# Optimization experiments

Hardware: AMD Instinct MI355X
Metric: run time of the kernel (lower is better)

The kernel has to match this reference:

```python
import jax, jax.numpy as jnp
import numpy as np

B, C, N, DI, DC = 64, 32, 1152, 8, 16
ROUTINGS = 3


def squash(x, axis=-1):
    sq = jnp.sum(x * x, axis=axis, keepdims=True)
    scale = sq / (1.0 + sq) / jnp.sqrt(sq + 1e-07)
    return scale * x


def setup_inputs() -> dict:
    key = jax.random.key(0)
    k1, k2 = jax.random.split(key)
    inputs = jax.random.normal(k1, (B, N, DI), dtype=jnp.float32)
    # Xavier-uniform init for W[n_caps, n_in, d_cap, d_in]; fan computed over last two dims
    limit = float(np.sqrt(6.0 / (DC + DI)))
    W = jax.random.uniform(k2, (C, N, DC, DI), dtype=jnp.float32, minval=-limit, maxval=limit)
    return {"inputs": inputs, "W": W}


def reference(inputs, W):
    # inputs_hat[b,c,n,i] = sum_j W[c,n,i,j] * inputs[b,n,j]
    inputs_hat = jnp.einsum('cnij,bnj->bcni', W, inputs)  # [B,C,N,DC]
    b = jnp.zeros((B, C, N), dtype=inputs_hat.dtype)
    outputs = None
    for i in range(ROUTINGS):
        c = jax.nn.softmax(b, axis=1)                      # over output capsules
        s = jnp.einsum('bcn,bcni->bci', c, inputs_hat)     # weighted sum over input caps
        outputs = squash(s)                                # [B,C,DC]
        if i < ROUTINGS - 1:
            agreement = jnp.einsum('bci,bcni->bcn', outputs, inputs_hat)
            b = b + agreement
    return outputs
```

## Files before the change

### kernel.cpp

```cpp
#include <hip/hip_runtime.h>
#include <hip/hip_fp16.h>

#define B_  64
#define C_  32
#define N_  1152
#define DI_ 8
#define DC_ 16
#define NCH 3
#define NSLOT 128
#define STH 512
#define NOCT 16

static __device__ __forceinline__ unsigned pkh(float a, float b) {
    __half2 t = __float22half2_rn(make_float2(a, b));
    return *reinterpret_cast<unsigned*>(&t);
}
static __device__ __forceinline__ float2 uph(unsigned u) {
    __half2 h; *reinterpret_cast<unsigned*>(&h) = u;
    return __half22float2(h);
}

__global__ __launch_bounds__(STH, 2) void caps_hat(
    const float* __restrict__ X, const float* __restrict__ W,
    uint4* __restrict__ hatg, float* __restrict__ p1)
{
    __shared__ float wlds[NCH * 64 * 64];
    __shared__ float xlds[NCH * 16 * 8];

    const int bg   = blockIdx.x & 3;
    const int slot = blockIdx.x >> 2;
    const int tid  = threadIdx.x;
    const int w    = tid >> 6;
    const int lane = tid & 63;
    const int c    = lane & 31;
    const int h    = lane >> 5;
    const int bl0  = w * 2;
    const int le   = 2 * c + h;
    const int sw   = c & 7;

    float acc[2][8];
#pragma unroll
    for (int bq = 0; bq < 2; bq++)
#pragma unroll
        for (int r = 0; r < 8; r++) acc[bq][r] = 0.f;

    for (int cc = 0; cc < 3; cc++) {
        if (cc) __syncthreads();
        const int n0 = (slot + cc * NSLOT) * NCH;

        for (int G = tid; G < NCH * 1024; G += STH) {
            const int nl = G >> 10, f = (G >> 4) & 63, q = G & 15;
            const int wc = f >> 1, wh = f & 1;
            const float4 v = *(const float4*)(W + (size_t)(wc * N_ + n0 + nl) * 128 + wh * 64 + q * 4);
            *(float4*)(wlds + (nl * 64 + f) * 64 + (q ^ (wc & 7)) * 4) = v;
        }
        if (tid < NCH * 32) {
            const int nl = tid >> 5, bl = (tid >> 1) & 15, qx = tid & 1;
            const float4 v = *(const float4*)(X + (size_t)((bg * 16 + bl) * N_ + n0 + nl) * DI_ + qx * 4);
            *(float4*)(xlds + (nl * 16 + bl) * 8 + qx * 4) = v;
        }
        __syncthreads();

#pragma unroll
        for (int nl = 0; nl < NCH; nl++) {
            float4 xa[2], xb[2];
#pragma unroll
            for (int bq = 0; bq < 2; bq++) {
                const float* xp = xlds + (nl * 16 + bl0 + bq) * 8;
                xa[bq] = *(const float4*)xp;
                xb[bq] = *(const float4*)(xp + 4);
            }
            uint4 hq[2];
            const float* frag = wlds + (nl * 64 + le) * 64;
#pragma unroll
            for (int rp = 0; rp < 4; rp++) {
                const int r0 = 2 * rp, r1 = r0 + 1;
                const int pa0 = ((2 * r0) ^ sw) * 4;
                const int pb0 = pa0 ^ 4;
                const int pa1 = ((2 * r1) ^ sw) * 4;
                const int pb1 = pa1 ^ 4;
                const float4 wa0 = *(const float4*)(frag + pa0);
                const float4 wb0 = *(const float4*)(frag + pb0);
                const float4 wa1 = *(const float4*)(frag + pa1);
                const float4 wb1 = *(const float4*)(frag + pb1);
#pragma unroll
                for (int bq = 0; bq < 2; bq++) {
                    const float hv0 = wa0.x*xa[bq].x + wa0.y*xa[bq].y + wa0.z*xa[bq].z + wa0.w*xa[bq].w
                                    + wb0.x*xb[bq].x + wb0.y*xb[bq].y + wb0.z*xb[bq].z + wb0.w*xb[bq].w;
                    const float hv1 = wa1.x*xa[bq].x + wa1.y*xa[bq].y + wa1.z*xa[bq].z + wa1.w*xa[bq].w
                                    + wb1.x*xb[bq].x + wb1.y*xb[bq].y + wb1.z*xb[bq].z + wb1.w*xb[bq].w;
                    acc[bq][r0] += hv0;
                    acc[bq][r1] += hv1;
                    (&hq[bq].x)[rp] = pkh(hv0, hv1);
                }
            }
#pragma unroll
            for (int bq = 0; bq < 2; bq++) {
                const int b = bg * 16 + bl0 + bq;
                hatg[(size_t)(b * N_ + n0 + nl) * 64 + le] = hq[bq];
            }
        }
    }

    float* pout = p1 + (size_t)(bg * NSLOT + slot) * 8192;
#pragma unroll
    for (int bq = 0; bq < 2; bq++) {
        float* pb = pout + (bl0 + bq) * 512 + le * 8;
        *(float4*)pb       = make_float4(acc[bq][0]*0.03125f, acc[bq][1]*0.03125f,
                                         acc[bq][2]*0.03125f, acc[bq][3]*0.03125f);
        *(float4*)(pb + 4) = make_float4(acc[bq][4]*0.03125f, acc[bq][5]*0.03125f,
                                         acc[bq][6]*0.03125f, acc[bq][7]*0.03125f);
    }
}

__global__ __launch_bounds__(STH, 2) void caps_route(
    const uint4* __restrict__ hatg, const float* __restrict__ accb,
    float* __restrict__ p2)
{
    __shared__ float red[8 * 512];
    const int b    = blockIdx.x >> 4;
    const int oct  = blockIdx.x & 15;
    const int tid  = threadIdx.x;
    const int w    = tid >> 6;
    const int lane = tid & 63;
    const int c    = lane & 31;
    const int h    = lane >> 5;
    const int le   = 2 * c + h;

    const float* ap = accb + (size_t)b * 512 + le * 8;
    const float4 a0 = *(const float4*)ap;
    const float4 a1 = *(const float4*)(ap + 4);

    float acc[8] = {0.f,0.f,0.f,0.f,0.f,0.f,0.f,0.f};
    const uint4* hb = hatg + (size_t)(b * N_ + oct * 72) * 64 + le;

    uint4 v[2][3];
#pragma unroll
    for (int u = 0; u < 3; u++)
        v[0][u] = hb[(size_t)(w + 8 * u) * 64];

#pragma unroll
    for (int k = 0; k < 3; k++) {
        const int cur = k & 1, nxt = cur ^ 1;
        if (k < 2) {
#pragma unroll
            for (int u = 0; u < 3; u++)
                v[nxt][u] = hb[(size_t)(w + 8 * (3 * (k + 1) + u)) * 64];
        }
#pragma unroll
        for (int u = 0; u < 3; u++) {
            const float2 f0 = uph(v[cur][u].x);
            const float2 f1 = uph(v[cur][u].y);
            const float2 f2 = uph(v[cur][u].z);
            const float2 f3 = uph(v[cur][u].w);
            float lg = f0.x*a0.x + f0.y*a0.y + f1.x*a0.z + f1.y*a0.w
                     + f2.x*a1.x + f2.y*a1.y + f3.x*a1.z + f3.y*a1.w;
            lg += __shfl_xor(lg, 32, 64);
            const float e = __expf(lg);
            float s = e;
#pragma unroll
            for (int m = 16; m >= 1; m >>= 1) s += __shfl_xor(s, m, 64);
            const float sc = e * __builtin_amdgcn_rcpf(s);
            acc[0] += sc * f0.x; acc[1] += sc * f0.y;
            acc[2] += sc * f1.x; acc[3] += sc * f1.y;
            acc[4] += sc * f2.x; acc[5] += sc * f2.y;
            acc[6] += sc * f3.x; acc[7] += sc * f3.y;
        }
    }
    *(float4*)(red + w * 512 + le * 8)     = make_float4(acc[0], acc[1], acc[2], acc[3]);
    *(float4*)(red + w * 512 + le * 8 + 4) = make_float4(acc[4], acc[5], acc[6], acc[7]);
    __syncthreads();
    float vs = 0.f;
#pragma unroll
    for (int s = 0; s < 8; s++) vs += red[s * 512 + tid];
    p2[(size_t)(b * NOCT + oct) * 512 + tid] = vs;
}

__global__ __launch_bounds__(256) void caps_r1(
    const float* __restrict__ p1, float* __restrict__ accb,
    float* __restrict__ out, int t)
{
    const int b   = blockIdx.x >> 2;
    const int q   = blockIdx.x & 3;
    const int tid = threadIdx.x;
    const int e   = q * 128 + (tid >> 1);
    const int p   = tid & 1;
    const int bg  = b >> 4, bl = b & 15;
    const float* base = p1 + (size_t)bg * NSLOT * 8192 + (size_t)bl * 512 + e;
    float v = 0.f;
#pragma unroll 8
    for (int ch = p; ch < NSLOT; ch += 2)
        v += base[(size_t)ch * 8192];
    v += __shfl_xor(v, 1, 64);
    float sq = v * v;
#pragma unroll
    for (int m = 2; m <= 16; m <<= 1) sq += __shfl_xor(sq, m, 64);
    const float scale = sq / (1.f + sq) * rsqrtf(sq + 1e-7f);
    const float ov = v * scale;
    if (p == 0) {
        const int oidx = b * 512 + e;
        if (t == 2) out[oidx] = ov;
        else        accb[oidx] = (t == 0) ? ov : (accb[oidx] + ov);
    }
}

__global__ __launch_bounds__(512) void caps_r2(
    const float* __restrict__ p2, float* __restrict__ accb,
    float* __restrict__ out, int t)
{
    const int b = blockIdx.x;
    const int e = threadIdx.x;
    const float* base = p2 + (size_t)b * (NOCT * 512) + e;
    float v = 0.f;
#pragma unroll
    for (int s = 0; s < NOCT; s++) v += base[s * 512];
    float sq = v * v;
#pragma unroll
    for (int m = 1; m <= 8; m <<= 1) sq += __shfl_xor(sq, m, 64);
    const float scale = sq / (1.f + sq) * rsqrtf(sq + 1e-7f);
    const float ov = v * scale;
    const int oidx = b * 512 + e;
    if (t == 2) out[oidx] = ov;
    else        accb[oidx] += ov;
}

__global__ __launch_bounds__(STH, 2) void caps_s_fb(
    const float* __restrict__ X, const float* __restrict__ W,
    const float* __restrict__ aout, float* __restrict__ partials, int t)
{
    __shared__ float wlds[NCH * 64 * 64];
    __shared__ float xlds[NCH * 16 * 8];
    const int bg = blockIdx.x & 3, slot = blockIdx.x >> 2;
    const int tid = threadIdx.x, w = tid >> 6, lane = tid & 63;
    const int c = lane & 31, h = lane >> 5, bl0 = w * 2, sw = c & 7;
    float areg[2][8] = {};
    if (t > 0) {
#pragma unroll
        for (int bq = 0; bq < 2; bq++) {
            const float* ap = aout + (size_t)(bg * 16 + bl0 + bq) * 512 + c * 16 + h * 8;
            const float4 a0 = *(const float4*)ap; const float4 a1 = *(const float4*)(ap + 4);
            areg[bq][0]=a0.x; areg[bq][1]=a0.y; areg[bq][2]=a0.z; areg[bq][3]=a0.w;
            areg[bq][4]=a1.x; areg[bq][5]=a1.y; areg[bq][6]=a1.z; areg[bq][7]=a1.w;
        }
    }
    float acc[2][8];
#pragma unroll
    for (int bq = 0; bq < 2; bq++)
#pragma unroll
        for (int r = 0; r < 8; r++) acc[bq][r] = 0.f;
    for (int cc = 0; cc < 3; cc++) {
        if (cc) __syncthreads();
        const int n0 = (slot + cc * NSLOT) * NCH;
        for (int G = tid; G < NCH * 1024; G += STH) {
            const int nl = G >> 10, f = (G >> 4) & 63, q = G & 15;
            const int wc = f >> 1, wh = f & 1;
            const float4 v = *(const float4*)(W + (size_t)(wc * N_ + n0 + nl) * 128 + wh * 64 + q * 4);
            *(float4*)(wlds + (nl * 64 + f) * 64 + (q ^ (wc & 7)) * 4) = v;
        }
        if (tid < NCH * 32) {
            const int nl = tid >> 5, bl = (tid >> 1) & 15, qx = tid & 1;
            const float4 v = *(const float4*)(X + (size_t)((bg * 16 + bl) * N_ + n0 + nl) * DI_ + qx * 4);
            *(float4*)(xlds + (nl * 16 + bl) * 8 + qx * 4) = v;
        }
        __syncthreads();
#pragma unroll
        for (int nl = 0; nl < NCH; nl++) {
            float4 xa[2], xb[2];
#pragma unroll
            for (int bq = 0; bq < 2; bq++) {
                const float* xp = xlds + (nl * 16 + bl0 + bq) * 8;
                xa[bq] = *(const float4*)xp; xb[bq] = *(const float4*)(xp + 4);
            }
            float hat[2][8];
            const float* frag = wlds + (nl * 64 + 2 * c + h) * 64;
#pragma unroll
            for (int r = 0; r < 8; r++) {
                const int pa = ((2 * r) ^ sw) * 4; const int pb = pa ^ 4;
                const float4 wa = *(const float4*)(frag + pa);
                const float4 wb = *(const float4*)(frag + pb);
#pragma unroll
                for (int bq = 0; bq < 2; bq++)
                    hat[bq][r] = wa.x*xa[bq].x + wa.y*xa[bq].y + wa.z*xa[bq].z + wa.w*xa[bq].w
                               + wb.x*xb[bq].x + wb.y*xb[bq].y + wb.z*xb[bq].z + wb.w*xb[bq].w;
            }
#pragma unroll
            for (int bq = 0; bq < 2; bq++) {
                float softc;
                if (t > 0) {
                    float lg = hat[bq][0]*areg[bq][0] + hat[bq][1]*areg[bq][1]
                             + hat[bq][2]*areg[bq][2] + hat[bq][3]*areg[bq][3]
                             + hat[bq][4]*areg[bq][4] + hat[bq][5]*areg[bq][5]
                             + hat[bq][6]*areg[bq][6] + hat[bq][7]*areg[bq][7];
                    lg += __shfl_xor(lg, 32, 64);
                    const float e = __expf(lg);
                    float s = e;
#pragma unroll
                    for (int m = 16; m >= 1; m >>= 1) s += __shfl_xor(s, m, 64);
                    softc = e / s;
                } else softc = 1.0f / 32.0f;
#pragma unroll
                for (int r = 0; r < 8; r++) acc[bq][r] += softc * hat[bq][r];
            }
        }
    }
    float* pout = partials + (size_t)(bg * NSLOT + slot) * 8192;
#pragma unroll
    for (int bq = 0; bq < 2; bq++) {
        float* pb = pout + (bl0 + bq) * 512 + c * 16 + h * 8;
        *(float4*)pb       = make_float4(acc[bq][0], acc[bq][1], acc[bq][2], acc[bq][3]);
        *(float4*)(pb + 4) = make_float4(acc[bq][4], acc[bq][5], acc[bq][6], acc[bq][7]);
    }
}

extern "C" void kernel_launch(void* const* d_in, const int* in_sizes, int n_in,
                              void* d_out, int out_size, void* d_ws, size_t ws_size,
                              hipStream_t stream) {
    const float* X = (const float*)d_in[0];
    const float* W = (const float*)d_in[1];
    float* out = (float*)d_out;

    const size_t hat_b = (size_t)B_ * N_ * 512 * 2;
    const size_t p1_b  = (size_t)512 * 8192 * 4;
    const size_t p2_b  = (size_t)B_ * NOCT * 512 * 4;
    const size_t acc_b = (size_t)B_ * 512 * 4;

    if (ws_size >= hat_b + p1_b + p2_b + acc_b) {
        char* ws = (char*)d_ws;
        uint4* hatg = (uint4*)ws;
        float* p1   = (float*)(ws + hat_b);
        float* p2   = (float*)(ws + hat_b + p1_b);
        float* accb = (float*)(ws + hat_b + p1_b + p2_b);
        caps_hat  <<<512, STH, 0, stream>>>(X, W, hatg, p1);
        caps_r1   <<<256, 256, 0, stream>>>(p1, accb, out, 0);
        caps_route<<<B_ * NOCT, STH, 0, stream>>>(hatg, accb, p2);
        caps_r2   <<<64, 512, 0, stream>>>(p2, accb, out, 1);
        caps_route<<<B_ * NOCT, STH, 0, stream>>>(hatg, accb, p2);
        caps_r2   <<<64, 512, 0, stream>>>(p2, accb, out, 2);
    } else {
        float* p1 = (float*)d_ws;
        float* accb = p1 + (size_t)512 * 8192;
        for (int t = 0; t < 3; t++) {
            caps_s_fb<<<512, STH, 0, stream>>>(X, W, accb, p1, t);
            caps_r1  <<<256, 256, 0, stream>>>(p1, accb, out, t);
        }
    }
}
```

Before: 140.0 us.

## Simplify hat kernel to per-input-capsule blocks and route first iteration from fp16 hat

The hat kernel is rewritten so each 64-thread block handles one input capsule, keeping its W slice in registers and looping over all 64 batches. It no longer writes the large fp32 partial-sum buffer. The first routing iteration now reuses the route kernel in a uniform-weight mode reading the stored fp16 hat, with a postscale of 1/32. This drops the p1 write and the reduction kernel in exchange for one extra pass over hat and a tiny-block launch of 1152 blocks. The route kernel also issues all nine loads up front instead of double-buffering them.

```diff
diff --git a/kernel.cpp b/kernel.cpp
--- a/kernel.cpp
+++ b/kernel.cpp
@@ -20,102 +20,51 @@
     return __half22float2(h);
 }
 
-__global__ __launch_bounds__(STH, 2) void caps_hat(
+__global__ __launch_bounds__(64) void caps_hat(
     const float* __restrict__ X, const float* __restrict__ W,
-    uint4* __restrict__ hatg, float* __restrict__ p1)
-{
-    __shared__ float wlds[NCH * 64 * 64];
-    __shared__ float xlds[NCH * 16 * 8];
-
-    const int bg   = blockIdx.x & 3;
-    const int slot = blockIdx.x >> 2;
-    const int tid  = threadIdx.x;
-    const int w    = tid >> 6;
-    const int lane = tid & 63;
+    uint4* __restrict__ hatg)
+{
+    __shared__ float xl[64 * 8];
+    const int n    = blockIdx.x;
+    const int lane = threadIdx.x;
     const int c    = lane & 31;
     const int h    = lane >> 5;
-    const int bl0  = w * 2;
-    const int le   = 2 * c + h;
-    const int sw   = c & 7;
-
-    float acc[2][8];
-#pragma unroll
-    for (int bq = 0; bq < 2; bq++)
-#pragma unroll
-        for (int r = 0; r < 8; r++) acc[bq][r] = 0.f;
-
-    for (int cc = 0; cc < 3; cc++) {
-        if (cc) __syncthreads();
-        const int n0 = (slot + cc * NSLOT) * NCH;
-
-        for (int G = tid; G < NCH * 1024; G += STH) {
-            const int nl = G >> 10, f = (G >> 4) & 63, q = G & 15;
-            const int wc = f >> 1, wh = f & 1;
-            const float4 v = *(const float4*)(W + (size_t)(wc * N_ + n0 + nl) * 128 + wh * 64 + q * 4);
-            *(float4*)(wlds + (nl * 64 + f) * 64 + (q ^ (wc & 7)) * 4) = v;
-        }
-        if (tid < NCH * 32) {
-            const int nl = tid >> 5, bl = (tid >> 1) & 15, qx = tid & 1;
-            const float4 v = *(const float4*)(X + (size_t)((bg * 16 + bl) * N_ + n0 + nl) * DI_ + qx * 4);
-            *(float4*)(xlds + (nl * 16 + bl) * 8 + qx * 4) = v;
-        }
-        __syncthreads();
-
-#pragma unroll
-        for (int nl = 0; nl < NCH; nl++) {
-            float4 xa[2], xb[2];
-#pragma unroll
-            for (int bq = 0; bq < 2; bq++) {
-                const float* xp = xlds + (nl * 16 + bl0 + bq) * 8;
-                xa[bq] = *(const float4*)xp;
-                xb[bq] = *(const float4*)(xp + 4);
-            }
-            uint4 hq[2];
-            const float* frag = wlds + (nl * 64 + le) * 64;
-#pragma unroll
-            for (int rp = 0; rp < 4; rp++) {
-                const int r0 = 2 * rp, r1 = r0 + 1;
-                const int pa0 = ((2 * r0) ^ sw) * 4;
-                const int pb0 = pa0 ^ 4;
-                const int pa1 = ((2 * r1) ^ sw) * 4;
-                const int pb1 = pa1 ^ 4;
-                const float4 wa0 = *(const float4*)(frag + pa0);
-                const float4 wb0 = *(const float4*)(frag + pb0);
-                const float4 wa1 = *(const float4*)(frag + pa1);
-                const float4 wb1 = *(const float4*)(frag + pb1);
-#pragma unroll
-                for (int bq = 0; bq < 2; bq++) {
-                    const float hv0 = wa0.x*xa[bq].x + wa0.y*xa[bq].y + wa0.z*xa[bq].z + wa0.w*xa[bq].w
-                                    + wb0.x*xb[bq].x + wb0.y*xb[bq].y + wb0.z*xb[bq].z + wb0.w*xb[bq].w;
-                    const float hv1 = wa1.x*xa[bq].x + wa1.y*xa[bq].y + wa1.z*xa[bq].z + wa1.w*xa[bq].w
-                                    + wb1.x*xb[bq].x + wb1.y*xb[bq].y + wb1.z*xb[bq].z + wb1.w*xb[bq].w;
-                    acc[bq][r0] += hv0;
-                    acc[bq][r1] += hv1;
-                    (&hq[bq].x)[rp] = pkh(hv0, hv1);
-                }
-            }
-#pragma unroll
-            for (int bq = 0; bq < 2; bq++) {
-                const int b = bg * 16 + bl0 + bq;
-                hatg[(size_t)(b * N_ + n0 + nl) * 64 + le] = hq[bq];
-            }
-        }
-    }
-
-    float* pout = p1 + (size_t)(bg * NSLOT + slot) * 8192;
-#pragma unroll
-    for (int bq = 0; bq < 2; bq++) {
-        float* pb = pout + (bl0 + bq) * 512 + le * 8;
-        *(float4*)pb       = make_float4(acc[bq][0]*0.03125f, acc[bq][1]*0.03125f,
-                                         acc[bq][2]*0.03125f, acc[bq][3]*0.03125f);
-        *(float4*)(pb + 4) = make_float4(acc[bq][4]*0.03125f, acc[bq][5]*0.03125f,
-                                         acc[bq][6]*0.03125f, acc[bq][7]*0.03125f);
+
+    {
+        const float* xp = X + ((size_t)lane * N_ + n) * 8;
+        *(float4*)(xl + lane * 8)     = *(const float4*)xp;
+        *(float4*)(xl + lane * 8 + 4) = *(const float4*)(xp + 4);
+    }
+    float4 wr[16];
+    const float* wp = W + ((size_t)c * N_ + n) * 128 + h * 64;
+#pragma unroll
+    for (int q = 0; q < 16; q++) wr[q] = *(const float4*)(wp + q * 4);
+    __syncthreads();
+
+    uint4* hout = hatg + (size_t)n * 64 + (2 * c + h);
+#pragma unroll 4
+    for (int b = 0; b < 64; b++) {
+        const float4 xa = *(const float4*)(xl + b * 8);
+        const float4 xb = *(const float4*)(xl + b * 8 + 4);
+        float hv[8];
+#pragma unroll
+        for (int r = 0; r < 8; r++) {
+            const float4 wa = wr[2 * r], wb = wr[2 * r + 1];
+            hv[r] = wa.x*xa.x + wa.y*xa.y + wa.z*xa.z + wa.w*xa.w
+                  + wb.x*xb.x + wb.y*xb.y + wb.z*xb.z + wb.w*xb.w;
+        }
+        uint4 hq;
+        hq.x = pkh(hv[0], hv[1]);
+        hq.y = pkh(hv[2], hv[3]);
+        hq.z = pkh(hv[4], hv[5]);
+        hq.w = pkh(hv[6], hv[7]);
+        hout[(size_t)b * (N_ * 64)] = hq;
     }
 }
 
 __global__ __launch_bounds__(STH, 2) void caps_route(
     const uint4* __restrict__ hatg, const float* __restrict__ accb,
-    float* __restrict__ p2)
+    float* __restrict__ p2, int mode, float postscale)
 {
     __shared__ float red[8 * 512];
     const int b    = blockIdx.x >> 4;
@@ -127,32 +76,28 @@
     const int h    = lane >> 5;
     const int le   = 2 * c + h;
 
-    const float* ap = accb + (size_t)b * 512 + le * 8;
-    const float4 a0 = *(const float4*)ap;
-    const float4 a1 = *(const float4*)(ap + 4);
+    float4 a0 = make_float4(0.f,0.f,0.f,0.f), a1 = a0;
+    if (mode) {
+        const float* ap = accb + (size_t)b * 512 + le * 8;
+        a0 = *(const float4*)ap;
+        a1 = *(const float4*)(ap + 4);
+    }
+
+    const uint4* hb = hatg + ((size_t)b * N_ + oct * 72) * 64 + le;
+    uint4 v[9];
+#pragma unroll
+    for (int idx = 0; idx < 9; idx++)
+        v[idx] = hb[(size_t)(w + 8 * idx) * 64];
 
     float acc[8] = {0.f,0.f,0.f,0.f,0.f,0.f,0.f,0.f};
-    const uint4* hb = hatg + (size_t)(b * N_ + oct * 72) * 64 + le;
-
-    uint4 v[2][3];
-#pragma unroll
-    for (int u = 0; u < 3; u++)
-        v[0][u] = hb[(size_t)(w + 8 * u) * 64];
-
-#pragma unroll
-    for (int k = 0; k < 3; k++) {
-        const int cur = k & 1, nxt = cur ^ 1;
-        if (k < 2) {
-#pragma unroll
-            for (int u = 0; u < 3; u++)
-                v[nxt][u] = hb[(size_t)(w + 8 * (3 * (k + 1) + u)) * 64];
-        }
-#pragma unroll
-        for (int u = 0; u < 3; u++) {
-            const float2 f0 = uph(v[cur][u].x);
-            const float2 f1 = uph(v[cur][u].y);
-            const float2 f2 = uph(v[cur][u].z);
-            const float2 f3 = uph(v[cur][u].w);
+#pragma unroll
+    for (int idx = 0; idx < 9; idx++) {
+        const float2 f0 = uph(v[idx].x);
+        const float2 f1 = uph(v[idx].y);
+        const float2 f2 = uph(v[idx].z);
+        const float2 f3 = uph(v[idx].w);
+        float sc;
+        if (mode) {
             float lg = f0.x*a0.x + f0.y*a0.y + f1.x*a0.z + f1.y*a0.w
                      + f2.x*a1.x + f2.y*a1.y + f3.x*a1.z + f3.y*a1.w;
             lg += __shfl_xor(lg, 32, 64);
@@ -160,23 +105,135 @@
             float s = e;
 #pragma unroll
             for (int m = 16; m >= 1; m >>= 1) s += __shfl_xor(s, m, 64);
-            const float sc = e * __builtin_amdgcn_rcpf(s);
-            acc[0] += sc * f0.x; acc[1] += sc * f0.y;
-            acc[2] += sc * f1.x; acc[3] += sc * f1.y;
-            acc[4] += sc * f2.x; acc[5] += sc * f2.y;
-            acc[6] += sc * f3.x; acc[7] += sc * f3.y;
-        }
-    }
+            sc = e * __builtin_amdgcn_rcpf(s);
+        } else {
+            sc = 1.0f;
+        }
+        acc[0] += sc * f0.x; acc[1] += sc * f0.y;
+        acc[2] += sc * f1.x; acc[3] += sc * f1.y;
+        acc[4] += sc * f2.x; acc[5] += sc * f2.y;
+        acc[6] += sc * f3.x; acc[7] += sc * f3.y;
+    }
+
     *(float4*)(red + w * 512 + le * 8)     = make_float4(acc[0], acc[1], acc[2], acc[3]);
     *(float4*)(red + w * 512 + le * 8 + 4) = make_float4(acc[4], acc[5], acc[6], acc[7]);
     __syncthreads();
     float vs = 0.f;
 #pragma unroll
     for (int s = 0; s < 8; s++) vs += red[s * 512 + tid];
-    p2[(size_t)(b * NOCT + oct) * 512 + tid] = vs;
-}
-
-__global__ __launch_bounds__(256) void caps_r1(
+    p2[(size_t)(b * NOCT + oct) * 512 + tid] = vs * postscale;
+}
+
+__global__ __launch_bounds__(512) void caps_r2(
+    const float* __restrict__ p2, float* __restrict__ accb,
+    float* __restrict__ out, int t)
+{
+    const int b = blockIdx.x;
+    const int e = threadIdx.x;
+    const float* base = p2 + (size_t)b * (NOCT * 512) + e;
+    float v = 0.f;
+#pragma unroll
+    for (int s = 0; s < NOCT; s++) v += base[s * 512];
+    float sq = v * v;
+#pragma unroll
+    for (int m = 1; m <= 8; m <<= 1) sq += __shfl_xor(sq, m, 64);
+    const float scale = sq / (1.f + sq) * rsqrtf(sq + 1e-7f);
+    const float ov = v * scale;
+    const int oidx = b * 512 + e;
+    if (t == 2)      out[oidx]  = ov;
+    else if (t == 0) accb[oidx] = ov;
+    else             accb[oidx] += ov;
+}
+
+__global__ __launch_bounds__(STH, 2) void caps_s_fb(
+    const float* __restrict__ X, const float* __restrict__ W,
+    const float* __restrict__ aout, float* __restrict__ partials, int t)
+{
+    __shared__ float wlds[NCH * 64 * 64];
+    __shared__ float xlds[NCH * 16 * 8];
+    const int bg = blockIdx.x & 3, slot = blockIdx.x >> 2;
+    const int tid = threadIdx.x, w = tid >> 6, lane = tid & 63;
+    const int c = lane & 31, h = lane >> 5, bl0 = w * 2, sw = c & 7;
+    float areg[2][8] = {};
+    if (t > 0) {
+#pragma unroll
+        for (int bq = 0; bq < 2; bq++) {
+            const float* ap = aout + (size_t)(bg * 16 + bl0 + bq) * 512 + c * 16 + h * 8;
+            const float4 a0 = *(const float4*)ap; const float4 a1 = *(const float4*)(ap + 4);
+            areg[bq][0]=a0.x; areg[bq][1]=a0.y; areg[bq][2]=a0.z; areg[bq][3]=a0.w;
+            areg[bq][4]=a1.x; areg[bq][5]=a1.y; areg[bq][6]=a1.z; areg[bq][7]=a1.w;
+        }
+    }
+    float acc[2][8];
+#pragma unroll
+    for (int bq = 0; bq < 2; bq++)
+#pragma unroll
+        for (int r = 0; r < 8; r++) acc[bq][r] = 0.f;
+    for (int cc = 0; cc < 3; cc++) {
+        if (cc) __syncthreads();
+        const int n0 = (slot + cc * NSLOT) * NCH;
+        for (int G = tid; G < NCH * 1024; G += STH) {
+            const int nl = G >> 10, f = (G >> 4) & 63, q = G & 15;
+            const int wc = f >> 1, wh = f & 1;
+            const float4 v = *(const float4*)(W + (size_t)(wc * N_ + n0 + nl) * 128 + wh * 64 + q * 4);
+            *(float4*)(wlds + (nl * 64 + f) * 64 + (q ^ (wc & 7)) * 4) = v;
+        }
+        if (tid < NCH * 32) {
+            const int nl = tid >> 5, bl = (tid >> 1) & 15, qx = tid & 1;
+            const float4 v = *(const float4*)(X + (size_t)((bg * 16 + bl) * N_ + n0 + nl) * DI_ + qx * 4);
+            *(float4*)(xlds + (nl * 16 + bl) * 8 + qx * 4) = v;
+        }
+        __syncthreads();
+#pragma unroll
+        for (int nl = 0; nl < NCH; nl++) {
+            float4 xa[2], xb[2];
+#pragma unroll
+            for (int bq = 0; bq < 2; bq++) {
+                const float* xp = xlds + (nl * 16 + bl0 + bq) * 8;
+                xa[bq] = *(const float4*)xp; xb[bq] = *(const float4*)(xp + 4);
+            }
+            float hat[2][8];
+            const float* frag = wlds + (nl * 64 + 2 * c + h) * 64;
+#pragma unroll
+            for (int r = 0; r < 8; r++) {
+                const int pa = ((2 * r) ^ sw) * 4; const int pb = pa ^ 4;
+                const float4 wa = *(const float4*)(frag + pa);
+                const float4 wb = *(const float4*)(frag + pb);
+#pragma unroll
+                for (int bq = 0; bq < 2; bq++)
+                    hat[bq][r] = wa.x*xa[bq].x + wa.y*xa[bq].y + wa.z*xa[bq].z + wa.w*xa[bq].w
+                               + wb.x*xb[bq].x + wb.y*xb[bq].y + wb.z*xb[bq].z + wb.w*xb[bq].w;
+            }
+#pragma unroll
+            for (int bq = 0; bq < 2; bq++) {
+                float softc;
+                if (t > 0) {
+                    float lg = hat[bq][0]*areg[bq][0] + hat[bq][1]*areg[bq][1]
+                             + hat[bq][2]*areg[bq][2] + hat[bq][3]*areg[bq][3]
+                             + hat[bq][4]*areg[bq][4] + hat[bq][5]*areg[bq][5]
+                             + hat[bq][6]*areg[bq][6] + hat[bq][7]*areg[bq][7];
+                    lg += __shfl_xor(lg, 32, 64);
+                    const float e = __expf(lg);
+                    float s = e;
+#pragma unroll
+                    for (int m = 16; m >= 1; m >>= 1) s += __shfl_xor(s, m, 64);
+                    softc = e / s;
+                } else softc = 1.0f / 32.0f;
+#pragma unroll
+                for (int r = 0; r < 8; r++) acc[bq][r] += softc * hat[bq][r];
+            }
+        }
+    }
+    float* pout = partials + (size_t)(bg * NSLOT + slot) * 8192;
+#pragma unroll
+    for (int bq = 0; bq < 2; bq++) {
+        float* pb = pout + (bl0 + bq) * 512 + c * 16 + h * 8;
+        *(float4*)pb       = make_float4(acc[bq][0], acc[bq][1], acc[bq][2], acc[bq][3]);
+        *(float4*)(pb + 4) = make_float4(acc[bq][4], acc[bq][5], acc[bq][6], acc[bq][7]);
+    }
+}
+
+__global__ __launch_bounds__(256) void caps_r1_fb(
     const float* __restrict__ p1, float* __restrict__ accb,
     float* __restrict__ out, int t)
 {
@@ -204,114 +261,6 @@
     }
 }
 
-__global__ __launch_bounds__(512) void caps_r2(
-    const float* __restrict__ p2, float* __restrict__ accb,
-    float* __restrict__ out, int t)
-{
-    const int b = blockIdx.x;
-    const int e = threadIdx.x;
-    const float* base = p2 + (size_t)b * (NOCT * 512) + e;
-    float v = 0.f;
-#pragma unroll
-    for (int s = 0; s < NOCT; s++) v += base[s * 512];
-    float sq = v * v;
-#pragma unroll
-    for (int m = 1; m <= 8; m <<= 1) sq += __shfl_xor(sq, m, 64);
-    const float scale = sq / (1.f + sq) * rsqrtf(sq + 1e-7f);
-    const float ov = v * scale;
-    const int oidx = b * 512 + e;
-    if (t == 2) out[oidx] = ov;
-    else        accb[oidx] += ov;
-}
-
-__global__ __launch_bounds__(STH, 2) void caps_s_fb(
-    const float* __restrict__ X, const float* __restrict__ W,
-    const float* __restrict__ aout, float* __restrict__ partials, int t)
-{
-    __shared__ float wlds[NCH * 64 * 64];
-    __shared__ float xlds[NCH * 16 * 8];
-    const int bg = blockIdx.x & 3, slot = blockIdx.x >> 2;
-    const int tid = threadIdx.x, w = tid >> 6, lane = tid & 63;
-    const int c = lane & 31, h = lane >> 5, bl0 = w * 2, sw = c & 7;
-    float areg[2][8] = {};
-    if (t > 0) {
-#pragma unroll
-        for (int bq = 0; bq < 2; bq++) {
-            const float* ap = aout + (size_t)(bg * 16 + bl0 + bq) * 512 + c * 16 + h * 8;
-            const float4 a0 = *(const float4*)ap; const float4 a1 = *(const float4*)(ap + 4);
-            areg[bq][0]=a0.x; areg[bq][1]=a0.y; areg[bq][2]=a0.z; areg[bq][3]=a0.w;
-            areg[bq][4]=a1.x; areg[bq][5]=a1.y; areg[bq][6]=a1.z; areg[bq][7]=a1.w;
-        }
-    }
-    float acc[2][8];
-#pragma unroll
-    for (int bq = 0; bq < 2; bq++)
-#pragma unroll
-        for (int r = 0; r < 8; r++) acc[bq][r] = 0.f;
-    for (int cc = 0; cc < 3; cc++) {
-        if (cc) __syncthreads();
-        const int n0 = (slot + cc * NSLOT) * NCH;
-        for (int G = tid; G < NCH * 1024; G += STH) {
-            const int nl = G >> 10, f = (G >> 4) & 63, q = G & 15;
-            const int wc = f >> 1, wh = f & 1;
-            const float4 v = *(const float4*)(W + (size_t)(wc * N_ + n0 + nl) * 128 + wh * 64 + q * 4);
-            *(float4*)(wlds + (nl * 64 + f) * 64 + (q ^ (wc & 7)) * 4) = v;
-        }
-        if (tid < NCH * 32) {
-            const int nl = tid >> 5, bl = (tid >> 1) & 15, qx = tid & 1;
-            const float4 v = *(const float4*)(X + (size_t)((bg * 16 + bl) * N_ + n0 + nl) * DI_ + qx * 4);
-            *(float4*)(xlds + (nl * 16 + bl) * 8 + qx * 4) = v;
-        }
-        __syncthreads();
-#pragma unroll
-        for (int nl = 0; nl < NCH; nl++) {
-            float4 xa[2], xb[2];
-#pragma unroll
-            for (int bq = 0; bq < 2; bq++) {
-                const float* xp = xlds + (nl * 16 + bl0 + bq) * 8;
-                xa[bq] = *(const float4*)xp; xb[bq] = *(const float4*)(xp + 4);
-            }
-            float hat[2][8];
-            const float* frag = wlds + (nl * 64 + 2 * c + h) * 64;
-#pragma unroll
-            for (int r = 0; r < 8; r++) {
-                const int pa = ((2 * r) ^ sw) * 4; const int pb = pa ^ 4;
-                const float4 wa = *(const float4*)(frag + pa);
-                const float4 wb = *(const float4*)(frag + pb);
-#pragma unroll
-                for (int bq = 0; bq < 2; bq++)
-                    hat[bq][r] = wa.x*xa[bq].x + wa.y*xa[bq].y + wa.z*xa[bq].z + wa.w*xa[bq].w
-                               + wb.x*xb[bq].x + wb.y*xb[bq].y + wb.z*xb[bq].z + wb.w*xb[bq].w;
-            }
-#pragma unroll
-            for (int bq = 0; bq < 2; bq++) {
-                float softc;
-                if (t > 0) {
-                    float lg = hat[bq][0]*areg[bq][0] + hat[bq][1]*areg[bq][1]
-                             + hat[bq][2]*areg[bq][2] + hat[bq][3]*areg[bq][3]
-                             + hat[bq][4]*areg[bq][4] + hat[bq][5]*areg[bq][5]
-                             + hat[bq][6]*areg[bq][6] + hat[bq][7]*areg[bq][7];
-                    lg += __shfl_xor(lg, 32, 64);
-                    const float e = __expf(lg);
-                    float s = e;
-#pragma unroll
-                    for (int m = 16; m >= 1; m >>= 1) s += __shfl_xor(s, m, 64);
-                    softc = e / s;
-                } else softc = 1.0f / 32.0f;
-#pragma unroll
-                for (int r = 0; r < 8; r++) acc[bq][r] += softc * hat[bq][r];
-            }
-        }
-    }
-    float* pout = partials + (size_t)(bg * NSLOT + slot) * 8192;
-#pragma unroll
-    for (int bq = 0; bq < 2; bq++) {
-        float* pb = pout + (bl0 + bq) * 512 + c * 16 + h * 8;
-        *(float4*)pb       = make_float4(acc[bq][0], acc[bq][1], acc[bq][2], acc[bq][3]);
-        *(float4*)(pb + 4) = make_float4(acc[bq][4], acc[bq][5], acc[bq][6], acc[bq][7]);
-    }
-}
-
 extern "C" void kernel_launch(void* const* d_in, const int* in_sizes, int n_in,
                               void* d_out, int out_size, void* d_ws, size_t ws_size,
                               hipStream_t stream) {
@@ -320,28 +269,27 @@
     float* out = (float*)d_out;
 
     const size_t hat_b = (size_t)B_ * N_ * 512 * 2;
-    const size_t p1_b  = (size_t)512 * 8192 * 4;
     const size_t p2_b  = (size_t)B_ * NOCT * 512 * 4;
     const size_t acc_b = (size_t)B_ * 512 * 4;
 
-    if (ws_size >= hat_b + p1_b + p2_b + acc_b) {
+    if (ws_size >= hat_b + p2_b + acc_b) {
         char* ws = (char*)d_ws;
         uint4* hatg = (uint4*)ws;
-        float* p1   = (float*)(ws + hat_b);
-        float* p2   = (float*)(ws + hat_b + p1_b);
-        float* accb = (float*)(ws + hat_b + p1_b + p2_b);
-        caps_hat  <<<512, STH, 0, stream>>>(X, W, hatg, p1);
-        caps_r1   <<<256, 256, 0, stream>>>(p1, accb, out, 0);
-        caps_route<<<B_ * NOCT, STH, 0, stream>>>(hatg, accb, p2);
-        caps_r2   <<<64, 512, 0, stream>>>(p2, accb, out, 1);
-        caps_route<<<B_ * NOCT, STH, 0, stream>>>(hatg, accb, p2);
-        caps_r2   <<<64, 512, 0, stream>>>(p2, accb, out, 2);
+        float* p2   = (float*)(ws + hat_b);
+        float* accb = (float*)(ws + hat_b + p2_b);
+        caps_hat  <<<N_, 64, 0, stream>>>(X, W, hatg);
+        caps_route<<<B_ * NOCT, STH, 0, stream>>>(hatg, accb, p2, 0, 0.03125f);
+        caps_r2   <<<B_, 512, 0, stream>>>(p2, accb, out, 0);
+        caps_route<<<B_ * NOCT, STH, 0, stream>>>(hatg, accb, p2, 1, 1.0f);
+        caps_r2   <<<B_, 512, 0, stream>>>(p2, accb, out, 1);
+        caps_route<<<B_ * NOCT, STH, 0, stream>>>(hatg, accb, p2, 1, 1.0f);
+        caps_r2   <<<B_, 512, 0, stream>>>(p2, accb, out, 2);
     } else {
         float* p1 = (float*)d_ws;
         float* accb = p1 + (size_t)512 * 8192;
         for (int t = 0; t < 3; t++) {
             caps_s_fb<<<512, STH, 0, stream>>>(X, W, accb, p1, t);
-            caps_r1  <<<256, 256, 0, stream>>>(p1, accb, out, t);
-        }
-    }
-}
+            caps_r1_fb<<<256, 256, 0, stream>>>(p1, accb, out, t);
+        }
+    }
+}
```

New measurement: 130.2 us. -7.0%, faster.
